# Optimization experiments

Hardware: AMD Instinct MI355X
Metric: run time of the kernel (lower is better)

## Reference

```python
import jax, jax.numpy as jnp
import numpy as np

N = 100_000   # nodes per type
E = 800_000   # edges per relation
H = 128       # hidden_channels
O = 64        # out_channels
TIME_SCALE = 1.0
LN_EPS = 1e-5


def setup_inputs() -> dict:
    key = jax.random.key(0)
    ks = jax.random.split(key, 24)
    nrm = lambda k, shp, s=1.0: jax.random.normal(k, shp, jnp.float32) * s
    inp = {}
    inp["x_A"] = nrm(ks[0], (N, H))
    inp["x_B"] = nrm(ks[1], (N, H))
    inp["x_C"] = nrm(ks[2], (N, H))
    inp["t_A"] = jax.random.uniform(ks[3], (N,), jnp.float32) * 1000.0
    inp["t_B"] = jax.random.uniform(ks[4], (N,), jnp.float32) * 1000.0
    inp["t_C"] = jax.random.uniform(ks[5], (N,), jnp.float32) * 1000.0
    inp["edge1"] = jnp.stack([jax.random.randint(ks[6], (E,), 0, N),
                              jax.random.randint(ks[7], (E,), 0, N)]).astype(jnp.int32)
    inp["edge2"] = jnp.stack([jax.random.randint(ks[8], (E,), 0, N),
                              jax.random.randint(ks[9], (E,), 0, N)]).astype(jnp.int32)
    kk = 10
    for i in range(2):
        inp[f"Wl{i}"] = nrm(ks[kk], (H, H), 0.05); kk += 1
        inp[f"bl{i}"] = jnp.zeros((H,), jnp.float32)
        inp[f"W0{i}"] = nrm(ks[kk], (H, H), 0.05); kk += 1
        inp[f"b0{i}"] = jnp.zeros((H,), jnp.float32)
        inp[f"W1{i}"] = nrm(ks[kk], (H, H), 0.05); kk += 1
        inp[f"b1{i}"] = jnp.zeros((H,), jnp.float32)
        inp[f"gate{i}"] = jnp.asarray(0.5, jnp.float32)
        inp[f"lam{i}"] = jnp.asarray(0.1, jnp.float32)  # raw lambda
        inp[f"lng{i}"] = jnp.ones((H,), jnp.float32)
        inp[f"lnb{i}"] = jnp.zeros((H,), jnp.float32)
    inp["Wout"] = nrm(ks[kk], (H, O), 0.05)
    inp["bout"] = jnp.zeros((O,), jnp.float32)
    return inp


def _layer(h_src, h_dst, x0_dst, edge, t_src, t_dst,
           Wl, bl, W0, b0, W1, b1, gate, raw_lam, lng, lnb):
    s, d = edge[0], edge[1]
    n_dst = h_dst.shape[0]
    # per-edge time-decay weight
    lam = jax.nn.softplus(raw_lam) + 1e-8
    delta = jnp.maximum((t_dst[d] - t_src[s]) / TIME_SCALE, 0.0)
    w = jnp.exp(jnp.maximum(-lam * delta, -60.0))          # [E]
    # gather + weight + scatter-add  (propagate with aggr='add')
    msg = h_src[s] * w[:, None]                            # [E,H]
    agg = jax.ops.segment_sum(msg, d, num_segments=n_dst)  # [n_dst,H]
    deg = jnp.maximum(jax.ops.segment_sum(w, d, num_segments=n_dst), 1e-6)
    out = agg / deg[:, None]
    g = jax.nn.sigmoid(gate)
    y = out @ Wl + bl + (1.0 - g) * (h_dst @ W0 + b0) + g * (x0_dst @ W1 + b1)
    y = jax.nn.relu(y)
    mu = jnp.mean(y, axis=-1, keepdims=True)
    var = jnp.mean((y - mu) ** 2, axis=-1, keepdims=True)
    y = (y - mu) * jax.lax.rsqrt(var + LN_EPS) * lng + lnb
    # index_copy_: only nodes that appear as a destination get updated
    cnt = jax.ops.segment_sum(jnp.ones_like(w), d, num_segments=n_dst)
    return jnp.where((cnt > 0)[:, None], y, h_dst)


def reference(x_A, x_B, x_C, t_A, t_B, t_C, edge1, edge2,
              Wl0, bl0, W00, b00, W10, b10, gate0, lam0, lng0, lnb0,
              Wl1, bl1, W01, b01, W11, b11, gate1, lam1, lng1, lnb1,
              Wout, bout):
    # reversed(metapath): process (B,r2,C) with conv_idx=1 first, then (A,r1,B) with conv_idx=0
    h_C = _layer(x_B, x_C, x_C, edge2, t_B, t_C,
                 Wl1, bl1, W01, b01, W11, b11, gate1, lam1, lng1, lnb1)
    h_B = _layer(x_A, x_B, x_B, edge1, t_A, t_B,
                 Wl0, bl0, W00, b00, W10, b10, gate0, lam0, lng0, lnb0)
    del h_B  # target type is metapath[-1][2] == 'C'; B's update does not feed C
    return h_C @ Wout + bout
```

## Files before the change

kernel.cpp:

```cpp
#include <hip/hip_runtime.h>


#define HD 128
#define OD 64
#define SCAN_E 1024

typedef unsigned short u16;
typedef short v8s __attribute__((ext_vector_type(8)));
typedef float v4f __attribute__((ext_vector_type(4)));

union Frag {
    unsigned int u[4];
    uint4 q;
    v8s v;
};

__device__ __forceinline__ float softplus_f(float x) {
    return fmaxf(x, 0.0f) + log1pf(expf(-fabsf(x)));
}
__device__ __forceinline__ float sigmoid_f(float x) {
    return 1.0f / (1.0f + expf(-x));
}
__device__ __forceinline__ int swz(int r, int c) {
    int g = (c >> 2) ^ (r & 7);
    return r * 128 + g * 4 + (c & 3);
}

__device__ __forceinline__ void split_store(float x, u16* ph, u16* pl) {
    unsigned int b = __float_as_uint(x);
    unsigned int h = b & 0xffff0000u;
    *ph = (u16)(h >> 16);
    float r = x - __uint_as_float(h);
    *pl = (u16)(__float_as_uint(r) >> 16);
}

__device__ __forceinline__ void cvt_split8(const float* f, unsigned int* hi,
                                           unsigned int* lo) {
#pragma unroll
    for (int j = 0; j < 4; ++j) {
        unsigned int b0 = __float_as_uint(f[2 * j]);
        unsigned int b1 = __float_as_uint(f[2 * j + 1]);
        unsigned int h0 = b0 & 0xffff0000u;
        unsigned int h1 = b1 & 0xffff0000u;
        hi[j] = (h0 >> 16) | h1;
        float r0 = f[2 * j]     - __uint_as_float(h0);
        float r1 = f[2 * j + 1] - __uint_as_float(h1);
        lo[j] = (__float_as_uint(r0) >> 16) | (__float_as_uint(r1) & 0xffff0000u);
    }
}

__global__ __launch_bounds__(256) void k_hist(
    const int* __restrict__ edge, int* __restrict__ cnt, int E)
{
    int e = blockIdx.x * 256 + threadIdx.x;
    if (e < E) atomicAdd(cnt + edge[E + e], 1);
}

__global__ __launch_bounds__(256) void k_scan1(
    const int* __restrict__ cnt, int* __restrict__ offs,
    int* __restrict__ part, int N)
{
    __shared__ int sh[256];
    const int t = threadIdx.x;
    const int base = blockIdx.x * SCAN_E + t * 4;
    int v[4], sum = 0;
#pragma unroll
    for (int i = 0; i < 4; ++i) {
        int idx = base + i;
        v[i] = (idx < N) ? cnt[idx] : 0;
        sum += v[i];
    }
    sh[t] = sum;
    __syncthreads();
    for (int off = 1; off < 256; off <<= 1) {
        int x = (t >= off) ? sh[t - off] : 0;
        __syncthreads();
        sh[t] += x;
        __syncthreads();
    }
    int run = (t > 0) ? sh[t - 1] : 0;
    if (t == 255) part[blockIdx.x] = sh[t];
#pragma unroll
    for (int i = 0; i < 4; ++i) {
        int idx = base + i;
        if (idx < N) offs[idx] = run;
        run += v[i];
    }
}

__global__ __launch_bounds__(128) void k_scan2(int* __restrict__ part, int NB)
{
    __shared__ int sh[128];
    const int t = threadIdx.x;
    sh[t] = (t < NB) ? part[t] : 0;
    __syncthreads();
    for (int off = 1; off < 128; off <<= 1) {
        int x = (t >= off) ? sh[t - off] : 0;
        __syncthreads();
        sh[t] += x;
        __syncthreads();
    }
    if (t < NB) part[t] = (t > 0) ? sh[t - 1] : 0;
}

__global__ __launch_bounds__(256) void k_fillw(
    const int* __restrict__ edge, const float* __restrict__ tB,
    const float* __restrict__ tC, const float* __restrict__ lam_raw,
    const int* __restrict__ offs, const int* __restrict__ part,
    int* __restrict__ fillc, int2* __restrict__ srcw, int E)
{
    int e = blockIdx.x * 256 + threadIdx.x;
    if (e >= E) return;
    int s = edge[e];
    int d = edge[E + e];
    float lam = softplus_f(lam_raw[0]) + 1e-8f;
    float dt  = fmaxf(tC[d] - tB[s], 0.0f);
    float w   = expf(fmaxf(-lam * dt, -60.0f));
    int pos = offs[d] + part[d >> 10] + atomicAdd(fillc + d, 1);
    srcw[pos] = make_int2(s, __float_as_int(w));
}

__global__ __launch_bounds__(256) void k_wprep(
    const float* __restrict__ Wl, const float* __restrict__ W0,
    const float* __restrict__ W1, const float* __restrict__ Wout,
    const float* __restrict__ bl, const float* __restrict__ b0,
    const float* __restrict__ b1, const float* __restrict__ gatep,
    u16* __restrict__ wlh, u16* __restrict__ wll,
    u16* __restrict__ wch, u16* __restrict__ wcl,
    u16* __restrict__ woh, u16* __restrict__ wol, float* __restrict__ bc)
{
    int i = blockIdx.x * 256 + threadIdx.x;
    const float g = sigmoid_f(gatep[0]);
    if (i < 16384) {
        int n = i >> 7, k = i & 127;
        float a  = Wl[k * 128 + n];
        float w0 = W0[k * 128 + n];
        float w1 = W1[k * 128 + n];
        float c  = (1.f - g) * w0 + g * w1;
        int off = ((k >> 5) * 128 + n) * 32 + (k & 31);
        split_store(a, wlh + off, wll + off);
        split_store(c, wch + off, wcl + off);
    } else if (i < 24576) {
        int j = i - 16384;
        int n = j >> 7, k = j & 127;
        float v = Wout[k * 64 + n];
        int off = ((k >> 5) * 64 + n) * 32 + (k & 31);
        split_store(v, woh + off, wol + off);
    } else if (i < 24704) {
        int t = i - 24576;
        bc[t] = bl[t] + (1.f - g) * b0[t] + g * b1[t];
    }
}

__global__ __launch_bounds__(256) void k_gather(
    const float* __restrict__ xB, const int2* __restrict__ srcw,
    const int* __restrict__ offs, const int* __restrict__ part,
    const int* __restrict__ cnt, float* __restrict__ aggn, int N)
{
    const int wave = (blockIdx.x * 256 + threadIdx.x) >> 6;
    const int lane = threadIdx.x & 63;
    const int slot = lane >> 4;
    const int l4   = lane & 15;
    if (wave >= N) return;
    const int r    = wave;
    const int degc = cnt[r];

    float* dstp = aggn + (size_t)r * HD;
    if (degc == 0) {
        if (slot == 0) {
            *reinterpret_cast<float4*>(dstp + l4 * 4) = make_float4(0, 0, 0, 0);
            *reinterpret_cast<float4*>(dstp + 64 + l4 * 4) = make_float4(0, 0, 0, 0);
        }
        return;
    }

    const int start = offs[r] + part[r >> 10];
    float4 a0 = make_float4(0, 0, 0, 0), a1 = make_float4(0, 0, 0, 0);
    float sw = 0.f;
#pragma unroll 2
    for (int j = slot; j < degc; j += 4) {
        int2 swp = srcw[start + j];
        float w = __int_as_float(swp.y);
        const float* row = xB + (size_t)swp.x * HD;
        float4 x0 = *reinterpret_cast<const float4*>(row + l4 * 4);
        float4 x1 = *reinterpret_cast<const float4*>(row + 64 + l4 * 4);
        a0.x = fmaf(w, x0.x, a0.x); a0.y = fmaf(w, x0.y, a0.y);
        a0.z = fmaf(w, x0.z, a0.z); a0.w = fmaf(w, x0.w, a0.w);
        a1.x = fmaf(w, x1.x, a1.x); a1.y = fmaf(w, x1.y, a1.y);
        a1.z = fmaf(w, x1.z, a1.z); a1.w = fmaf(w, x1.w, a1.w);
        sw += w;
    }
#pragma unroll
    for (int m = 16; m <= 32; m <<= 1) {
        a0.x += __shfl_xor(a0.x, m); a0.y += __shfl_xor(a0.y, m);
        a0.z += __shfl_xor(a0.z, m); a0.w += __shfl_xor(a0.w, m);
        a1.x += __shfl_xor(a1.x, m); a1.y += __shfl_xor(a1.y, m);
        a1.z += __shfl_xor(a1.z, m); a1.w += __shfl_xor(a1.w, m);
        sw   += __shfl_xor(sw, m);
    }
    float inv = 1.0f / fmaxf(sw, 1e-6f);
    if (slot == 0) {
        a0.x *= inv; a0.y *= inv; a0.z *= inv; a0.w *= inv;
        a1.x *= inv; a1.y *= inv; a1.z *= inv; a1.w *= inv;
        *reinterpret_cast<float4*>(dstp + l4 * 4) = a0;
        *reinterpret_cast<float4*>(dstp + 64 + l4 * 4) = a1;
    }
}

__global__ __launch_bounds__(256) void k_fused(
    const float* __restrict__ xC, const float* __restrict__ aggn,
    const int* __restrict__ cnt,
    const u16* __restrict__ wlh, const u16* __restrict__ wll,
    const u16* __restrict__ wch, const u16* __restrict__ wcl,
    const u16* __restrict__ woh, const u16* __restrict__ wol,
    const float* __restrict__ bc, const float* __restrict__ lng,
    const float* __restrict__ lnb, const float* __restrict__ bout,
    float* __restrict__ out, int N)
{
    __shared__ float lds[4 * 16 * 128];

    const int lane = threadIdx.x & 63;
    const int wid  = threadIdx.x >> 6;
    const int lr   = lane & 15;
    const int kb   = lane >> 4;
    const int row0 = blockIdx.x * 128 + wid * 32;
    float* myl = lds + wid * 16 * 128;

    v4f acc[2][8] = {};

#pragma unroll
    for (int mat = 0; mat < 2; ++mat) {
        const float* Asrc = mat ? xC : aggn;
        const uint4* BH = (const uint4*)(mat ? wch : wlh);
        const uint4* BL = (const uint4*)(mat ? wcl : wll);
#pragma unroll
        for (int kc = 0; kc < 4; ++kc) {
            Frag ah[2], al[2];
#pragma unroll
            for (int rt = 0; rt < 2; ++rt) {
                int r = row0 + rt * 16 + lr;
                r = (r < N) ? r : (N - 1);
                const float4* ap = (const float4*)(
                    Asrc + (size_t)r * HD + kc * 32 + kb * 8);
                float4 u0 = ap[0], u1 = ap[1];
                float f[8] = {u0.x, u0.y, u0.z, u0.w, u1.x, u1.y, u1.z, u1.w};
                cvt_split8(f, ah[rt].u, al[rt].u);
            }
#pragma unroll
            for (int ct = 0; ct < 8; ++ct) {
                int idx = kc * 512 + (ct * 16 + lr) * 4 + kb;
                Frag bh, bl;
                bh.q = BH[idx];
                bl.q = BL[idx];
#pragma unroll
                for (int rt = 0; rt < 2; ++rt) {
                    acc[rt][ct] = __builtin_amdgcn_mfma_f32_16x16x32_bf16(
                        ah[rt].v, bh.v, acc[rt][ct], 0, 0, 0);
                    acc[rt][ct] = __builtin_amdgcn_mfma_f32_16x16x32_bf16(
                        ah[rt].v, bl.v, acc[rt][ct], 0, 0, 0);
                    acc[rt][ct] = __builtin_amdgcn_mfma_f32_16x16x32_bf16(
                        al[rt].v, bh.v, acc[rt][ct], 0, 0, 0);
                }
            }
        }
    }

    float bcv[8], gav[8], bev[8];
#pragma unroll
    for (int ct = 0; ct < 8; ++ct) {
        int c = ct * 16 + lr;
        bcv[ct] = bc[c];
        gav[ct] = lng[c];
        bev[ct] = lnb[c];
    }
    float bov[4];
#pragma unroll
    for (int ct = 0; ct < 4; ++ct) bov[ct] = bout[ct * 16 + lr];

    const uint4* BH3 = (const uint4*)woh;
    const uint4* BL3 = (const uint4*)wol;

#pragma unroll
    for (int rt = 0; rt < 2; ++rt) {
        int rq = row0 + rt * 16 + kb * 4;
        int cvr[4] = {0, 0, 0, 0};
        if (rq < N) {
            int4 cv = *(const int4*)(cnt + rq);
            cvr[0] = cv.x; cvr[1] = cv.y; cvr[2] = cv.z; cvr[3] = cv.w;
        }
#pragma unroll
        for (int reg = 0; reg < 4; ++reg) {
            int rloc = kb * 4 + reg;
            int r    = rq + reg;
            float yv[8];
            float s = 0.f, q = 0.f;
#pragma unroll
            for (int ct = 0; ct < 8; ++ct) {
                float v = acc[rt][ct][reg] + bcv[ct];
                v = fmaxf(v, 0.0f);
                yv[ct] = v;
                s += v;
                q += v * v;
            }
#pragma unroll
            for (int m = 1; m < 16; m <<= 1) {
                s += __shfl_xor(s, m);
                q += __shfl_xor(q, m);
            }
            float mu   = s * (1.0f / 128.0f);
            float var  = q * (1.0f / 128.0f) - mu * mu;
            float rstd = rsqrtf(var + 1e-5f);

            if (r < N) {
                if (cvr[reg] > 0) {
#pragma unroll
                    for (int ct = 0; ct < 8; ++ct)
                        myl[swz(rloc, ct * 16 + lr)] =
                            (yv[ct] - mu) * rstd * gav[ct] + bev[ct];
                } else {
                    size_t base = (size_t)r * HD;
#pragma unroll
                    for (int ct = 0; ct < 8; ++ct)
                        myl[swz(rloc, ct * 16 + lr)] = xC[base + ct * 16 + lr];
                }
            } else {
#pragma unroll
                for (int ct = 0; ct < 8; ++ct)
                    myl[swz(rloc, ct * 16 + lr)] = 0.0f;
            }
        }

        v4f acc2[4] = {};
#pragma unroll
        for (int kc = 0; kc < 4; ++kc) {
            Frag ah, al;
            {
                int c0 = kc * 32 + kb * 8;
                float4 u0 = *reinterpret_cast<const float4*>(&myl[swz(lr, c0)]);
                float4 u1 = *reinterpret_cast<const float4*>(&myl[swz(lr, c0 + 4)]);
                float f[8] = {u0.x, u0.y, u0.z, u0.w, u1.x, u1.y, u1.z, u1.w};
                cvt_split8(f, ah.u, al.u);
            }
#pragma unroll
            for (int ct = 0; ct < 4; ++ct) {
                int idx = kc * 256 + (ct * 16 + lr) * 4 + kb;
                Frag bh, bl;
                bh.q = BH3[idx];
                bl.q = BL3[idx];
                acc2[ct] = __builtin_amdgcn_mfma_f32_16x16x32_bf16(
                    ah.v, bh.v, acc2[ct], 0, 0, 0);
                acc2[ct] = __builtin_amdgcn_mfma_f32_16x16x32_bf16(
                    ah.v, bl.v, acc2[ct], 0, 0, 0);
                acc2[ct] = __builtin_amdgcn_mfma_f32_16x16x32_bf16(
                    al.v, bh.v, acc2[ct], 0, 0, 0);
            }
        }

#pragma unroll
        for (int reg = 0; reg < 4; ++reg) {
            int r = rq + reg;
            if (r < N) {
#pragma unroll
                for (int ct = 0; ct < 4; ++ct)
                    out[(size_t)r * OD + ct * 16 + lr] = acc2[ct][reg] + bov[ct];
            }
        }
    }
}

extern "C" void kernel_launch(void* const* d_in, const int* in_sizes, int n_in,
                              void* d_out, int out_size, void* d_ws, size_t ws_size,
                              hipStream_t stream) {
    const float* xB    = (const float*)d_in[1];
    const float* xC    = (const float*)d_in[2];
    const float* tB    = (const float*)d_in[4];
    const float* tC    = (const float*)d_in[5];
    const int*   edge2 = (const int*)d_in[7];
    const float* Wl1   = (const float*)d_in[18];
    const float* bl1   = (const float*)d_in[19];
    const float* W01   = (const float*)d_in[20];
    const float* b01   = (const float*)d_in[21];
    const float* W11   = (const float*)d_in[22];
    const float* b11   = (const float*)d_in[23];
    const float* gate1 = (const float*)d_in[24];
    const float* lam1  = (const float*)d_in[25];
    const float* lng1  = (const float*)d_in[26];
    const float* lnb1  = (const float*)d_in[27];
    const float* Wout  = (const float*)d_in[28];
    const float* bout  = (const float*)d_in[29];

    const int N = in_sizes[2] / HD;
    const int E = in_sizes[7] / 2;

    int*   cnt   = (int*)d_ws;
    int*   fillc = cnt + N;
    int*   offs  = fillc + N;
    int*   part  = offs + N;
    int2*  srcw  = (int2*)(part + 128);
    u16*   wlh   = (u16*)(srcw + E);
    u16*   wll   = wlh + 16384;
    u16*   wch   = wll + 16384;
    u16*   wcl   = wch + 16384;
    u16*   woh   = wcl + 16384;
    u16*   wol   = woh + 8192;
    float* bc    = (float*)(wol + 8192);
    float* buf   = bc + 128;

    hipMemsetAsync(cnt, 0, (size_t)2 * N * sizeof(int), stream);

    dim3 blk(256);
    const int gE = (E + 255) / 256;
    const int NB = (N + SCAN_E - 1) / SCAN_E;

    k_wprep<<<97, blk, 0, stream>>>(Wl1, W01, W11, Wout, bl1, b01, b11, gate1,
                                    wlh, wll, wch, wcl, woh, wol, bc);
    k_hist <<<gE, blk, 0, stream>>>(edge2, cnt, E);
    k_scan1<<<NB, blk, 0, stream>>>(cnt, offs, part, N);
    k_scan2<<<1, 128, 0, stream>>>(part, NB);
    k_fillw<<<gE, blk, 0, stream>>>(edge2, tB, tC, lam1, offs, part, fillc, srcw, E);

    const int gN64 = (N * 64 + 255) / 256;
    k_gather<<<gN64, blk, 0, stream>>>(xB, srcw, offs, part, cnt, buf, N);

    const int GB = (N + 127) / 128;
    k_fused<<<GB, blk, 0, stream>>>(xC, buf, cnt, wlh, wll, wch, wcl, woh, wol,
                                    bc, lng1, lnb1, bout, (float*)d_out, N);
}
```

Before: 223.0 us.

## Merge histogram into weight prep, replace second scan with atomics, halve fused tile

The histogram kernel is merged into the weight-prep kernel so one launch covers both. The second scan pass is dropped: each scan block takes its base offset through an atomicAdd on a running total. Because blocks can grab that total out of order, edge segments are no longer laid out in node order, but each node's offset stays consistent. The fused MFMA kernel now handles 16 rows per wave instead of 32, doubling the block count to raise occupancy at the cost of more reloads of the B fragments.

```diff
diff --git a/kernel.cpp b/kernel.cpp
--- a/kernel.cpp
+++ b/kernel.cpp
@@ -49,78 +49,8 @@
     }
 }
 
-__global__ __launch_bounds__(256) void k_hist(
-    const int* __restrict__ edge, int* __restrict__ cnt, int E)
-{
-    int e = blockIdx.x * 256 + threadIdx.x;
-    if (e < E) atomicAdd(cnt + edge[E + e], 1);
-}
-
-__global__ __launch_bounds__(256) void k_scan1(
-    const int* __restrict__ cnt, int* __restrict__ offs,
-    int* __restrict__ part, int N)
-{
-    __shared__ int sh[256];
-    const int t = threadIdx.x;
-    const int base = blockIdx.x * SCAN_E + t * 4;
-    int v[4], sum = 0;
-#pragma unroll
-    for (int i = 0; i < 4; ++i) {
-        int idx = base + i;
-        v[i] = (idx < N) ? cnt[idx] : 0;
-        sum += v[i];
-    }
-    sh[t] = sum;
-    __syncthreads();
-    for (int off = 1; off < 256; off <<= 1) {
-        int x = (t >= off) ? sh[t - off] : 0;
-        __syncthreads();
-        sh[t] += x;
-        __syncthreads();
-    }
-    int run = (t > 0) ? sh[t - 1] : 0;
-    if (t == 255) part[blockIdx.x] = sh[t];
-#pragma unroll
-    for (int i = 0; i < 4; ++i) {
-        int idx = base + i;
-        if (idx < N) offs[idx] = run;
-        run += v[i];
-    }
-}
-
-__global__ __launch_bounds__(128) void k_scan2(int* __restrict__ part, int NB)
-{
-    __shared__ int sh[128];
-    const int t = threadIdx.x;
-    sh[t] = (t < NB) ? part[t] : 0;
-    __syncthreads();
-    for (int off = 1; off < 128; off <<= 1) {
-        int x = (t >= off) ? sh[t - off] : 0;
-        __syncthreads();
-        sh[t] += x;
-        __syncthreads();
-    }
-    if (t < NB) part[t] = (t > 0) ? sh[t - 1] : 0;
-}
-
-__global__ __launch_bounds__(256) void k_fillw(
-    const int* __restrict__ edge, const float* __restrict__ tB,
-    const float* __restrict__ tC, const float* __restrict__ lam_raw,
-    const int* __restrict__ offs, const int* __restrict__ part,
-    int* __restrict__ fillc, int2* __restrict__ srcw, int E)
-{
-    int e = blockIdx.x * 256 + threadIdx.x;
-    if (e >= E) return;
-    int s = edge[e];
-    int d = edge[E + e];
-    float lam = softplus_f(lam_raw[0]) + 1e-8f;
-    float dt  = fmaxf(tC[d] - tB[s], 0.0f);
-    float w   = expf(fmaxf(-lam * dt, -60.0f));
-    int pos = offs[d] + part[d >> 10] + atomicAdd(fillc + d, 1);
-    srcw[pos] = make_int2(s, __float_as_int(w));
-}
-
-__global__ __launch_bounds__(256) void k_wprep(
+__global__ __launch_bounds__(256) void k_prep(
+    const int* __restrict__ edge, int* __restrict__ cnt, int E, int gE,
     const float* __restrict__ Wl, const float* __restrict__ W0,
     const float* __restrict__ W1, const float* __restrict__ Wout,
     const float* __restrict__ bl, const float* __restrict__ b0,
@@ -129,7 +59,12 @@
     u16* __restrict__ wch, u16* __restrict__ wcl,
     u16* __restrict__ woh, u16* __restrict__ wol, float* __restrict__ bc)
 {
-    int i = blockIdx.x * 256 + threadIdx.x;
+    if (blockIdx.x < (unsigned)gE) {
+        int e = blockIdx.x * 256 + threadIdx.x;
+        if (e < E) atomicAdd(cnt + edge[E + e], 1);
+        return;
+    }
+    int i = (blockIdx.x - gE) * 256 + threadIdx.x;
     const float g = sigmoid_f(gatep[0]);
     if (i < 16384) {
         int n = i >> 7, k = i & 127;
@@ -152,6 +87,55 @@
     }
 }
 
+__global__ __launch_bounds__(256) void k_scan1(
+    const int* __restrict__ cnt, int* __restrict__ offs,
+    int* __restrict__ part, int* __restrict__ tot, int N)
+{
+    __shared__ int sh[256];
+    const int t = threadIdx.x;
+    const int base = blockIdx.x * SCAN_E + t * 4;
+    int v[4], sum = 0;
+#pragma unroll
+    for (int i = 0; i < 4; ++i) {
+        int idx = base + i;
+        v[i] = (idx < N) ? cnt[idx] : 0;
+        sum += v[i];
+    }
+    sh[t] = sum;
+    __syncthreads();
+    for (int off = 1; off < 256; off <<= 1) {
+        int x = (t >= off) ? sh[t - off] : 0;
+        __syncthreads();
+        sh[t] += x;
+        __syncthreads();
+    }
+    int run = (t > 0) ? sh[t - 1] : 0;
+    if (t == 255) part[blockIdx.x] = atomicAdd(tot, sh[255]);
+#pragma unroll
+    for (int i = 0; i < 4; ++i) {
+        int idx = base + i;
+        if (idx < N) offs[idx] = run;
+        run += v[i];
+    }
+}
+
+__global__ __launch_bounds__(256) void k_fillw(
+    const int* __restrict__ edge, const float* __restrict__ tB,
+    const float* __restrict__ tC, const float* __restrict__ lam_raw,
+    const int* __restrict__ offs, const int* __restrict__ part,
+    int* __restrict__ fillc, int2* __restrict__ srcw, int E)
+{
+    int e = blockIdx.x * 256 + threadIdx.x;
+    if (e >= E) return;
+    int s = edge[e];
+    int d = edge[E + e];
+    float lam = softplus_f(lam_raw[0]) + 1e-8f;
+    float dt  = fmaxf(tC[d] - tB[s], 0.0f);
+    float w   = expf(fmaxf(-lam * dt, -60.0f));
+    int pos = offs[d] + part[d >> 10] + atomicAdd(fillc + d, 1);
+    srcw[pos] = make_int2(s, __float_as_int(w));
+}
+
 __global__ __launch_bounds__(256) void k_gather(
     const float* __restrict__ xB, const int2* __restrict__ srcw,
     const int* __restrict__ offs, const int* __restrict__ part,
@@ -223,10 +207,10 @@
     const int wid  = threadIdx.x >> 6;
     const int lr   = lane & 15;
     const int kb   = lane >> 4;
-    const int row0 = blockIdx.x * 128 + wid * 32;
+    const int row0 = blockIdx.x * 64 + wid * 16;
     float* myl = lds + wid * 16 * 128;
 
-    v4f acc[2][8] = {};
+    v4f acc[8] = {};
 
 #pragma unroll
     for (int mat = 0; mat < 2; ++mat) {
@@ -235,16 +219,15 @@
         const uint4* BL = (const uint4*)(mat ? wcl : wll);
 #pragma unroll
         for (int kc = 0; kc < 4; ++kc) {
-            Frag ah[2], al[2];
-#pragma unroll
-            for (int rt = 0; rt < 2; ++rt) {
-                int r = row0 + rt * 16 + lr;
+            Frag ah, al;
+            {
+                int r = row0 + lr;
                 r = (r < N) ? r : (N - 1);
                 const float4* ap = (const float4*)(
                     Asrc + (size_t)r * HD + kc * 32 + kb * 8);
                 float4 u0 = ap[0], u1 = ap[1];
                 float f[8] = {u0.x, u0.y, u0.z, u0.w, u1.x, u1.y, u1.z, u1.w};
-                cvt_split8(f, ah[rt].u, al[rt].u);
+                cvt_split8(f, ah.u, al.u);
             }
 #pragma unroll
             for (int ct = 0; ct < 8; ++ct) {
@@ -252,15 +235,12 @@
                 Frag bh, bl;
                 bh.q = BH[idx];
                 bl.q = BL[idx];
-#pragma unroll
-                for (int rt = 0; rt < 2; ++rt) {
-                    acc[rt][ct] = __builtin_amdgcn_mfma_f32_16x16x32_bf16(
-                        ah[rt].v, bh.v, acc[rt][ct], 0, 0, 0);
-                    acc[rt][ct] = __builtin_amdgcn_mfma_f32_16x16x32_bf16(
-                        ah[rt].v, bl.v, acc[rt][ct], 0, 0, 0);
-                    acc[rt][ct] = __builtin_amdgcn_mfma_f32_16x16x32_bf16(
-                        al[rt].v, bh.v, acc[rt][ct], 0, 0, 0);
-                }
+                acc[ct] = __builtin_amdgcn_mfma_f32_16x16x32_bf16(
+                    ah.v, bh.v, acc[ct], 0, 0, 0);
+                acc[ct] = __builtin_amdgcn_mfma_f32_16x16x32_bf16(
+                    ah.v, bl.v, acc[ct], 0, 0, 0);
+                acc[ct] = __builtin_amdgcn_mfma_f32_16x16x32_bf16(
+                    al.v, bh.v, acc[ct], 0, 0, 0);
             }
         }
     }
@@ -273,16 +253,9 @@
         gav[ct] = lng[c];
         bev[ct] = lnb[c];
     }
-    float bov[4];
-#pragma unroll
-    for (int ct = 0; ct < 4; ++ct) bov[ct] = bout[ct * 16 + lr];
-
-    const uint4* BH3 = (const uint4*)woh;
-    const uint4* BL3 = (const uint4*)wol;
-
-#pragma unroll
-    for (int rt = 0; rt < 2; ++rt) {
-        int rq = row0 + rt * 16 + kb * 4;
+
+    {
+        int rq = row0 + kb * 4;
         int cvr[4] = {0, 0, 0, 0};
         if (rq < N) {
             int4 cv = *(const int4*)(cnt + rq);
@@ -296,7 +269,7 @@
             float s = 0.f, q = 0.f;
 #pragma unroll
             for (int ct = 0; ct < 8; ++ct) {
-                float v = acc[rt][ct][reg] + bcv[ct];
+                float v = acc[ct][reg] + bcv[ct];
                 v = fmaxf(v, 0.0f);
                 yv[ct] = v;
                 s += v;
@@ -329,41 +302,48 @@
                     myl[swz(rloc, ct * 16 + lr)] = 0.0f;
             }
         }
-
-        v4f acc2[4] = {};
-#pragma unroll
-        for (int kc = 0; kc < 4; ++kc) {
-            Frag ah, al;
-            {
-                int c0 = kc * 32 + kb * 8;
-                float4 u0 = *reinterpret_cast<const float4*>(&myl[swz(lr, c0)]);
-                float4 u1 = *reinterpret_cast<const float4*>(&myl[swz(lr, c0 + 4)]);
-                float f[8] = {u0.x, u0.y, u0.z, u0.w, u1.x, u1.y, u1.z, u1.w};
-                cvt_split8(f, ah.u, al.u);
-            }
-#pragma unroll
-            for (int ct = 0; ct < 4; ++ct) {
-                int idx = kc * 256 + (ct * 16 + lr) * 4 + kb;
-                Frag bh, bl;
-                bh.q = BH3[idx];
-                bl.q = BL3[idx];
-                acc2[ct] = __builtin_amdgcn_mfma_f32_16x16x32_bf16(
-                    ah.v, bh.v, acc2[ct], 0, 0, 0);
-                acc2[ct] = __builtin_amdgcn_mfma_f32_16x16x32_bf16(
-                    ah.v, bl.v, acc2[ct], 0, 0, 0);
-                acc2[ct] = __builtin_amdgcn_mfma_f32_16x16x32_bf16(
-                    al.v, bh.v, acc2[ct], 0, 0, 0);
-            }
-        }
-
-#pragma unroll
-        for (int reg = 0; reg < 4; ++reg) {
-            int r = rq + reg;
-            if (r < N) {
-#pragma unroll
-                for (int ct = 0; ct < 4; ++ct)
-                    out[(size_t)r * OD + ct * 16 + lr] = acc2[ct][reg] + bov[ct];
-            }
+    }
+
+    v4f acc2[4] = {};
+    const uint4* BH3 = (const uint4*)woh;
+    const uint4* BL3 = (const uint4*)wol;
+
+#pragma unroll
+    for (int kc = 0; kc < 4; ++kc) {
+        Frag ah, al;
+        {
+            int c0 = kc * 32 + kb * 8;
+            float4 u0 = *reinterpret_cast<const float4*>(&myl[swz(lr, c0)]);
+            float4 u1 = *reinterpret_cast<const float4*>(&myl[swz(lr, c0 + 4)]);
+            float f[8] = {u0.x, u0.y, u0.z, u0.w, u1.x, u1.y, u1.z, u1.w};
+            cvt_split8(f, ah.u, al.u);
+        }
+#pragma unroll
+        for (int ct = 0; ct < 4; ++ct) {
+            int idx = kc * 256 + (ct * 16 + lr) * 4 + kb;
+            Frag bh, bl;
+            bh.q = BH3[idx];
+            bl.q = BL3[idx];
+            acc2[ct] = __builtin_amdgcn_mfma_f32_16x16x32_bf16(
+                ah.v, bh.v, acc2[ct], 0, 0, 0);
+            acc2[ct] = __builtin_amdgcn_mfma_f32_16x16x32_bf16(
+                ah.v, bl.v, acc2[ct], 0, 0, 0);
+            acc2[ct] = __builtin_amdgcn_mfma_f32_16x16x32_bf16(
+                al.v, bh.v, acc2[ct], 0, 0, 0);
+        }
+    }
+
+    float bov[4];
+#pragma unroll
+    for (int ct = 0; ct < 4; ++ct) bov[ct] = bout[ct * 16 + lr];
+
+#pragma unroll
+    for (int reg = 0; reg < 4; ++reg) {
+        int r = row0 + kb * 4 + reg;
+        if (r < N) {
+#pragma unroll
+            for (int ct = 0; ct < 4; ++ct)
+                out[(size_t)r * OD + ct * 16 + lr] = acc2[ct][reg] + bov[ct];
         }
     }
 }
@@ -396,7 +376,8 @@
     int*   fillc = cnt + N;
     int*   offs  = fillc + N;
     int*   part  = offs + N;
-    int2*  srcw  = (int2*)(part + 128);
+    int*   tot   = part + 128;
+    int2*  srcw  = (int2*)(tot + 4);
     u16*   wlh   = (u16*)(srcw + E);
     u16*   wll   = wlh + 16384;
     u16*   wch   = wll + 16384;
@@ -407,22 +388,22 @@
     float* buf   = bc + 128;
 
     hipMemsetAsync(cnt, 0, (size_t)2 * N * sizeof(int), stream);
+    hipMemsetAsync(tot, 0, sizeof(int), stream);
 
     dim3 blk(256);
     const int gE = (E + 255) / 256;
     const int NB = (N + SCAN_E - 1) / SCAN_E;
 
-    k_wprep<<<97, blk, 0, stream>>>(Wl1, W01, W11, Wout, bl1, b01, b11, gate1,
-                                    wlh, wll, wch, wcl, woh, wol, bc);
-    k_hist <<<gE, blk, 0, stream>>>(edge2, cnt, E);
-    k_scan1<<<NB, blk, 0, stream>>>(cnt, offs, part, N);
-    k_scan2<<<1, 128, 0, stream>>>(part, NB);
+    k_prep <<<gE + 97, blk, 0, stream>>>(edge2, cnt, E, gE,
+                                         Wl1, W01, W11, Wout, bl1, b01, b11,
+                                         gate1, wlh, wll, wch, wcl, woh, wol, bc);
+    k_scan1<<<NB, blk, 0, stream>>>(cnt, offs, part, tot, N);
     k_fillw<<<gE, blk, 0, stream>>>(edge2, tB, tC, lam1, offs, part, fillc, srcw, E);
 
     const int gN64 = (N * 64 + 255) / 256;
     k_gather<<<gN64, blk, 0, stream>>>(xB, srcw, offs, part, cnt, buf, N);
 
-    const int GB = (N + 127) / 128;
+    const int GB = (N + 63) / 64;
     k_fused<<<GB, blk, 0, stream>>>(xC, buf, cnt, wlh, wll, wch, wcl, woh, wol,
                                     bc, lng1, lnb1, bout, (float*)d_out, N);
 }
```

After: 240.6 us. 7.9% more time.
